# Performance work log

Measured on AMD Instinct MI355X. Metric: run time of the kernel, lower is better.

## Reference

```python
import jax, jax.numpy as jnp
import numpy as np

POS = np.array([[0,3,0.5],[0,3,1.5],[0,3,2.5],[0,3,3.5],[0,3,4.5],[0,3,5.5],[1,0,0],[1,6,6],[2,0,6],[2,6,0],[3,0,0],[3,6,6],[4,0,6],[4,6,0],[5,0,0],[5,6,6],[6,0,6],[6,6,0],[7,0,0],[7,6,6],[8,0,6],[8,6,0],[9,0,0],[9,6,6],[10,0,6],[10,6,0],[11,0,0],[11,6,6],[12,0,6],[12,6,0],[13,0,0],[13,6,6],[14,0,6],[14,6,0],[15,0,0],[15,6,6],[16,0,6],[16,6,0],[17,0.5,0.5],[17,3,0.5],[17,5.5,0.5],[17,0.5,3],[17,3,3],[17,5.5,3],[17,0.5,5.5],[17,3,5.5],[17,5.5,5.5]], dtype=np.float32)  # (47,3) fixed buffer

B, S, D, H, FF, HID = 512, 47, 32, 4, 2048, 256

def _ln(x, w, b, eps=1e-5):
    mu = jnp.mean(x, -1, keepdims=True)
    var = jnp.mean((x - mu) ** 2, -1, keepdims=True)
    return (x - mu) * jax.lax.rsqrt(var + eps) * w + b

def _encoder_layer(h, wi, bi, wo, bo, l1w, l1b, f1w, f1b, f2w, f2b, l2w, l2b):
    # torch post-norm TransformerEncoderLayer; batch_first=False => attention over axis 0
    L, N, E = h.shape
    Dh = E // H
    qkv = h @ wi.T + bi                                  # (L,N,3E)
    q, k, v = jnp.split(qkv, 3, axis=-1)
    q = q.reshape(L, N, H, Dh); k = k.reshape(L, N, H, Dh); v = v.reshape(L, N, H, Dh)
    scores = jnp.einsum('lnhd,mnhd->nhlm', q, k) * (1.0 / np.sqrt(Dh))  # (N,H,L,L)
    a = jax.nn.softmax(scores, axis=-1)
    o = jnp.einsum('nhlm,mnhd->lnhd', a, v).reshape(L, N, E)
    h = _ln(h + (o @ wo.T + bo), l1w, l1b)
    ff = jax.nn.relu(h @ f1w.T + f1b) @ f2w.T + f2b
    return _ln(h + ff, l2w, l2b)

def setup_inputs():
    key = jax.random.key(0)
    ks = list(jax.random.split(key, 24))
    rn = lambda k, s, sc=0.05: jax.random.normal(k, s, jnp.float32) * sc
    return dict(
        x=jax.random.normal(ks[0], (B, S), jnp.float32),
        w_in=rn(ks[1], (D, 1)), b_in=rn(ks[2], (D,)),
        w_pos=rn(ks[3], (D, 3)), b_pos=rn(ks[4], (D,)),
        cls_token=rn(ks[5], (1, 1, D), 1.0),
        attn_in_w=rn(ks[6], (2, 3 * D, D)), attn_in_b=rn(ks[7], (2, 3 * D)),
        attn_out_w=rn(ks[8], (2, D, D)), attn_out_b=rn(ks[9], (2, D)),
        ln1_w=jnp.ones((2, D)), ln1_b=jnp.zeros((2, D)),
        ff1_w=rn(ks[10], (2, FF, D)), ff1_b=rn(ks[11], (2, FF)),
        ff2_w=rn(ks[12], (2, D, FF)), ff2_b=rn(ks[13], (2, D)),
        ln2_w=jnp.ones((2, D)), ln2_b=jnp.zeros((2, D)),
        out_w=rn(ks[14], (1, D)), out_b=rn(ks[15], (1,)),
        mlp_w0=rn(ks[16], (HID, S)), mlp_b0=rn(ks[17], (HID,)),
        mlp_w1=rn(ks[18], (HID, HID)), mlp_b1=rn(ks[19], (HID,)),
        mlp_w2=rn(ks[20], (1, HID)), mlp_b2=rn(ks[21], (1,)),
    )

def reference(x, w_in, b_in, w_pos, b_pos, cls_token, attn_in_w, attn_in_b, attn_out_w, attn_out_b, ln1_w, ln1_b, ff1_w, ff1_b, ff2_w, ff2_b, ln2_w, ln2_b, out_w, out_b, mlp_w0, mlp_b0, mlp_w1, mlp_b1, mlp_w2, mlp_b2):
    Bn = x.shape[0]
    h = x[..., None] * w_in[:, 0] + b_in                 # Linear(1,D): (B,S,D)
    h = h + (jnp.asarray(POS) @ w_pos.T + b_pos)         # pos projection (S,D)
    cls = jnp.broadcast_to(cls_token, (Bn, 1, D))
    h = jnp.concatenate([cls, h], axis=1)                # (B,S+1,D)
    for i in range(2):
        h = _encoder_layer(h, attn_in_w[i], attn_in_b[i], attn_out_w[i], attn_out_b[i], ln1_w[i], ln1_b[i], ff1_w[i], ff1_b[i], ff2_w[i], ff2_b[i], ln2_w[i], ln2_b[i])
    out = jax.nn.relu(h[:, 1:, :] @ out_w.T + out_b)[..., 0]   # (B,S); dropout = eval identity
    o = jax.nn.relu(out @ mlp_w0.T + mlp_b0)
    o = jax.nn.relu(o @ mlp_w1.T + mlp_b1)
    o = jax.nn.relu(o @ mlp_w2.T + mlp_b2)               # MLP ends with ReLU per source
    return o
```

## Files before the change

### kernel.cpp

```cpp
#include <hip/hip_runtime.h>

#define NB 512
#define NS 47
#define NP 48
#define DIM 32
#define NFF 2048
#define NHID 256
#define NROWS (NB * NP)
#define FTOK 48

#define VSTR 520
#define PSTR 72
#define USTR 136

typedef _Float16 f16x8 __attribute__((ext_vector_type(8)));
typedef _Float16 f16x4 __attribute__((ext_vector_type(4)));
typedef float f32x4 __attribute__((ext_vector_type(4)));

__constant__ float POSC[NS * 3] = {
  0,3,0.5f, 0,3,1.5f, 0,3,2.5f, 0,3,3.5f, 0,3,4.5f, 0,3,5.5f,
  1,0,0, 1,6,6, 2,0,6, 2,6,0, 3,0,0, 3,6,6, 4,0,6, 4,6,0,
  5,0,0, 5,6,6, 6,0,6, 6,6,0, 7,0,0, 7,6,6, 8,0,6, 8,6,0,
  9,0,0, 9,6,6, 10,0,6, 10,6,0, 11,0,0, 11,6,6, 12,0,6, 12,6,0,
  13,0,0, 13,6,6, 14,0,6, 14,6,0, 15,0,0, 15,6,6, 16,0,6, 16,6,0,
  17,0.5f,0.5f, 17,3,0.5f, 17,5.5f,0.5f, 17,0.5f,3, 17,3,3, 17,5.5f,3,
  17,0.5f,5.5f, 17,3,5.5f, 17,5.5f,5.5f
};

__global__ __launch_bounds__(256) void prep16_kernel(const float* __restrict__ w1,
                                                     const float* __restrict__ w2,
                                                     _Float16* __restrict__ w1h,
                                                     _Float16* __restrict__ w2h) {
  int idx = blockIdx.x * 256 + threadIdx.x;
  w1h[idx] = (_Float16)w1[idx];
  w2h[idx] = (_Float16)w2[idx];
}

__global__ __launch_bounds__(256) void embed_kernel(
    const float* __restrict__ x, const float* __restrict__ w_in, const float* __restrict__ b_in,
    const float* __restrict__ w_pos, const float* __restrict__ b_pos,
    const float* __restrict__ cls, float* __restrict__ h) {
  int idx = blockIdx.x * 256 + threadIdx.x;
  int r = idx >> 5, d = idx & 31;
  int l = r / NP, n = r - l * NP;
  float v;
  if (n == 0) {
    v = cls[d];
  } else {
    int s = n - 1;
    v = x[l * NS + s] * w_in[d] + b_in[d]
      + POSC[s * 3 + 0] * w_pos[d * 3 + 0]
      + POSC[s * 3 + 1] * w_pos[d * 3 + 1]
      + POSC[s * 3 + 2] * w_pos[d * 3 + 2] + b_pos[d];
  }
  h[idx] = v;
}

__global__ __launch_bounds__(256) void kv_kernel(
    const float* __restrict__ h, const float* __restrict__ wi, const float* __restrict__ bi,
    _Float16* __restrict__ Kp, _Float16* __restrict__ Vt) {
  __shared__ float ws_[512];
  __shared__ float bs_[16];
  const int t = threadIdx.x;
  const int nh = blockIdx.x >> 1;
  const int n = nh >> 2, hh = nh & 3;
  const int l = ((blockIdx.x & 1) << 8) | t;
  for (int i = t; i < 512; i += 256) {
    int sub = i >> 8, rem = i & 255;
    int jj = rem >> 5, d = rem & 31;
    ws_[i] = wi[((sub + 1) * 32 + hh * 8 + jj) * 32 + d];
  }
  if (t < 16) bs_[t] = bi[((t >> 3) + 1) * 32 + hh * 8 + (t & 7)];
  __syncthreads();
  const float4* hrow = (const float4*)(h + (l * NP + n) * 32);
  float4 hv[8];
  #pragma unroll
  for (int i = 0; i < 8; ++i) hv[i] = hrow[i];
  f16x8 kh, kl_, vh;
  #pragma unroll
  for (int jj = 0; jj < 8; ++jj) {
    float k0 = bs_[jj], k1 = 0.f, k2 = 0.f, k3 = 0.f;
    float v0 = bs_[8 + jj], v1 = 0.f, v2 = 0.f, v3 = 0.f;
    #pragma unroll
    for (int d4 = 0; d4 < 8; ++d4) {
      float4 hvv = hv[d4];
      k0 += hvv.x * ws_[jj * 32 + 4 * d4 + 0];
      k1 += hvv.y * ws_[jj * 32 + 4 * d4 + 1];
      k2 += hvv.z * ws_[jj * 32 + 4 * d4 + 2];
      k3 += hvv.w * ws_[jj * 32 + 4 * d4 + 3];
      v0 += hvv.x * ws_[256 + jj * 32 + 4 * d4 + 0];
      v1 += hvv.y * ws_[256 + jj * 32 + 4 * d4 + 1];
      v2 += hvv.z * ws_[256 + jj * 32 + 4 * d4 + 2];
      v3 += hvv.w * ws_[256 + jj * 32 + 4 * d4 + 3];
    }
    float kv = (k0 + k1) + (k2 + k3);
    float vv = (v0 + v1) + (v2 + v3);
    kh[jj] = (_Float16)kv; kl_[jj] = (_Float16)(kv - (float)kh[jj]);
    vh[jj] = (_Float16)vv;
  }
  _Float16* kdst = Kp + ((size_t)nh * 512 + l) * 16;
  *(f16x8*)(kdst) = kh;
  *(f16x8*)(kdst + 8) = kl_;
  #pragma unroll
  for (int d = 0; d < 8; ++d) Vt[(size_t)nh * 4096 + d * 512 + l] = vh[d];
}

__global__ __launch_bounds__(256, 2) void attn_mfma_kernel(
    const float* __restrict__ h, const float* __restrict__ wi, const float* __restrict__ bi,
    const _Float16* __restrict__ Kp, const _Float16* __restrict__ Vt,
    float* __restrict__ o) {
  __shared__ alignas(16) _Float16 khi[512 * 8];
  __shared__ alignas(16) _Float16 klo[512 * 8];
  __shared__ alignas(16) _Float16 vts[8 * VSTR];
  __shared__ alignas(16) float hq_pls[4608];
  __shared__ alignas(16) _Float16 qf[128 * 16];
  __shared__ float wsq[256];
  __shared__ float bq[8];
  const int bx = blockIdx.x;
  const int nh = bx >> 2, qc = bx & 3;
  const int n = nh >> 2, hh = nh & 3;
  const int t = threadIdx.x;
  const int lane = t & 63, wv = t >> 6;
  const int c = lane & 15, g = lane >> 4;

  const _Float16* kg = Kp + (size_t)nh * 8192;
  for (int r = t; r < 512; r += 256) {
    const uint4* src = (const uint4*)(kg + r * 16);
    uint4 a = src[0], b = src[1];
    *(uint4*)(khi + r * 8) = a;
    *(uint4*)(klo + r * 8) = b;
  }
  {
    const _Float16* vg = Vt + (size_t)nh * 4096;
    for (int i = t; i < 512; i += 256) {
      int d = i >> 6, seg = i & 63;
      *(uint4*)(vts + d * VSTR + seg * 8) = *(const uint4*)(vg + d * 512 + seg * 8);
    }
  }
  wsq[t] = wi[(hh * 8 + (t & 7)) * 32 + (t >> 3)];
  if (t < 8) bq[t] = bi[hh * 8 + t];
  float* hq = hq_pls;

  #pragma unroll
  for (int rp = 0; rp < 2; ++rp) {
    {
      int row = t >> 2, quar = t & 3;
      const float4* src =
          (const float4*)(h + (((qc * 128 + rp * 64 + row) * NP) + n) * 32 + quar * 8);
      float4 a = src[0], b = src[1];
      __syncthreads();
      *(float4*)(hq + row * 36 + quar * 8) = a;
      *(float4*)(hq + row * 36 + quar * 8 + 4) = b;
    }
    __syncthreads();
    {
      int row = t >> 2, pr = t & 3;
      #pragma unroll
      for (int u = 0; u < 2; ++u) {
        int jj = pr * 2 + u;
        float a = bq[jj];
        #pragma unroll
        for (int d = 0; d < 32; ++d) a += hq[row * 36 + d] * wsq[d * 8 + jj];
        _Float16 qh = (_Float16)a;
        _Float16 ql = (_Float16)(a - (float)qh);
        qf[(rp * 64 + row) * 16 + jj] = qh;
        qf[(rp * 64 + row) * 16 + 8 + jj] = ql;
      }
    }
    __syncthreads();
  }

  const f16x8 hz = {(_Float16)0,(_Float16)0,(_Float16)0,(_Float16)0,
                    (_Float16)0,(_Float16)0,(_Float16)0,(_Float16)0};
  const f32x4 zf = {0.f, 0.f, 0.f, 0.f};
  _Float16* pls_ = (_Float16*)hq_pls;
  _Float16* mypA = pls_ + wv * (16 * PSTR);
  _Float16* mypB = pls_ + (4 + wv) * (16 * PSTR);
  const int q0A = qc * 128 + wv * 16;
  const int q0B = q0A + 64;

  f16x8 aqA = hz, aqB = hz;
  if (g < 3) {
    aqA = *(const f16x8*)(qf + (wv * 16 + c) * 16 + (g & 1) * 8);
    aqB = *(const f16x8*)(qf + (64 + wv * 16 + c) * 16 + (g & 1) * 8);
  }
  f32x4 accA = {0.f, 0.f, 0.f, 0.f}, accB = {0.f, 0.f, 0.f, 0.f};
  float lsA[4] = {0.f, 0.f, 0.f, 0.f}, lsB[4] = {0.f, 0.f, 0.f, 0.f};

  for (int ch = 0; ch < 8; ++ch) {
    const int kb = ch * 64;
    #pragma unroll
    for (int kt = 0; kt < 4; ++kt) {
      f16x8 bk = hz;
      if (g < 2)       bk = *(const f16x8*)(khi + (kb + kt * 16 + c) * 8);
      else if (g == 2) bk = *(const f16x8*)(klo + (kb + kt * 16 + c) * 8);
      f32x4 sA = __builtin_amdgcn_mfma_f32_16x16x32_f16(aqA, bk, zf, 0, 0, 0);
      f32x4 sB = __builtin_amdgcn_mfma_f32_16x16x32_f16(aqB, bk, zf, 0, 0, 0);
      #pragma unroll
      for (int r = 0; r < 4; ++r) {
        float pA = __expf(sA[r] * 0.35355339059327373f - 2.0f);
        float pB = __expf(sB[r] * 0.35355339059327373f - 2.0f);
        _Float16 phA = (_Float16)pA;
        _Float16 phB = (_Float16)pB;
        lsA[r] += (float)phA;
        lsB[r] += (float)phB;
        mypA[(g * 4 + r) * PSTR + kt * 16 + c] = phA;
        mypB[(g * 4 + r) * PSTR + kt * 16 + c] = phB;
      }
    }
    #pragma unroll
    for (int half = 0; half < 2; ++half) {
      f16x8 bv = hz;
      if (c < 8) bv = *(const f16x8*)(vts + c * VSTR + kb + half * 32 + g * 8);
      f16x8 apA = *(const f16x8*)(mypA + c * PSTR + half * 32 + g * 8);
      f16x8 apB = *(const f16x8*)(mypB + c * PSTR + half * 32 + g * 8);
      accA = __builtin_amdgcn_mfma_f32_16x16x32_f16(apA, bv, accA, 0, 0, 0);
      accB = __builtin_amdgcn_mfma_f32_16x16x32_f16(apB, bv, accB, 0, 0, 0);
    }
  }
  #pragma unroll
  for (int m = 1; m < 16; m <<= 1) {
    #pragma unroll
    for (int r = 0; r < 4; ++r) {
      lsA[r] += __shfl_xor(lsA[r], m, 64);
      lsB[r] += __shfl_xor(lsB[r], m, 64);
    }
  }
  if (c < 8) {
    #pragma unroll
    for (int r = 0; r < 4; ++r) {
      o[((q0A + g * 4 + r) * NP + n) * 32 + hh * 8 + c] = accA[r] / lsA[r];
      o[((q0B + g * 4 + r) * NP + n) * 32 + hh * 8 + c] = accB[r] / lsB[r];
    }
  }
}

__global__ __launch_bounds__(256) void proj_ln1_kernel(
    const float* __restrict__ o, const float* __restrict__ wo, const float* __restrict__ bo,
    const float* __restrict__ lw, const float* __restrict__ lb, float* __restrict__ h) {
  __shared__ float wos[32 * 33];
  __shared__ float pre[64 * 33];
  const int g = blockIdx.x, t = threadIdx.x;
  for (int i = t; i < 1024; i += 256) wos[(i >> 5) * 33 + (i & 31)] = wo[i];
  __syncthreads();
  const int subr = t >> 2, jq = t & 3;
  const int r = g * 64 + subr;
  const float4* orow = (const float4*)(o + r * 32);
  float4 ov[8];
  #pragma unroll
  for (int i = 0; i < 8; ++i) ov[i] = orow[i];
  const float* hres = h + r * 32 + jq * 8;
  #pragma unroll
  for (int jj = 0; jj < 8; ++jj) {
    int j = jq * 8 + jj;
    float a0 = bo[j], a1 = 0.f, a2 = 0.f, a3 = 0.f;
    #pragma unroll
    for (int d4 = 0; d4 < 8; ++d4) {
      float4 vv = ov[d4];
      a0 += vv.x * wos[j * 33 + 4 * d4 + 0];
      a1 += vv.y * wos[j * 33 + 4 * d4 + 1];
      a2 += vv.z * wos[j * 33 + 4 * d4 + 2];
      a3 += vv.w * wos[j * 33 + 4 * d4 + 3];
    }
    pre[subr * 33 + j] = (a0 + a1) + (a2 + a3) + hres[jj];
  }
  __syncthreads();
  if (t < 64) {
    float mu = 0.f;
    #pragma unroll
    for (int d = 0; d < 32; ++d) mu += pre[t * 33 + d];
    mu *= (1.f / 32.f);
    float var = 0.f;
    #pragma unroll
    for (int d = 0; d < 32; ++d) { float dv = pre[t * 33 + d] - mu; var += dv * dv; }
    float rs = rsqrtf(var * (1.f / 32.f) + 1e-5f);
    float* hrow = h + (g * 64 + t) * 32;
    #pragma unroll
    for (int d = 0; d < 32; ++d)
      hrow[d] = (pre[t * 33 + d] - mu) * rs * lw[d] + lb[d];
  }
}

__global__ __launch_bounds__(256) void ff_fused_kernel(
    const float* __restrict__ h, const _Float16* __restrict__ w1h,
    const float* __restrict__ b1, const _Float16* __restrict__ w2h,
    const float* __restrict__ b2, const float* __restrict__ lw,
    const float* __restrict__ lb, const float* __restrict__ ow,
    const float* __restrict__ ob, float* __restrict__ svec, int do_svec) {
  __shared__ alignas(16) _Float16 ubuf[4][2][16 * USTR];
  __shared__ alignas(16) float yw[4][FTOK * 33];
  const int t = threadIdx.x;
  const int lane = t & 63;
  const int wv = t >> 6;
  const int nl = lane & 15;
  const int g = lane >> 4;
  const int g4 = g * 4;
  const int r0 = blockIdx.x * FTOK;

  f16x8 hfrag[3];
  #pragma unroll
  for (int tt = 0; tt < 3; ++tt) {
    const float4 h0 = *(const float4*)(h + (r0 + tt * 16 + nl) * 32 + g * 8);
    const float4 h1 = *(const float4*)(h + (r0 + tt * 16 + nl) * 32 + g * 8 + 4);
    hfrag[tt][0] = (_Float16)h0.x; hfrag[tt][1] = (_Float16)h0.y;
    hfrag[tt][2] = (_Float16)h0.z; hfrag[tt][3] = (_Float16)h0.w;
    hfrag[tt][4] = (_Float16)h1.x; hfrag[tt][5] = (_Float16)h1.y;
    hfrag[tt][6] = (_Float16)h1.z; hfrag[tt][7] = (_Float16)h1.w;
  }

  f32x4 acc0[3] = {{0.f,0.f,0.f,0.f},{0.f,0.f,0.f,0.f},{0.f,0.f,0.f,0.f}};
  f32x4 acc1[3] = {{0.f,0.f,0.f,0.f},{0.f,0.f,0.f,0.f},{0.f,0.f,0.f,0.f}};
  const f32x4 zero = {0.f, 0.f, 0.f, 0.f};
  const int ffbase = wv * 512;

  #pragma unroll
  for (int sc = 0; sc < 4; ++sc) {
    const int ffb = ffbase + sc * 128;
    f16x8 wf[8];
    float4 bv[8];
    #pragma unroll
    for (int ft = 0; ft < 8; ++ft) {
      wf[ft] = *(const f16x8*)(w1h + (ffb + ft * 16 + nl) * 32 + g * 8);
      bv[ft] = *(const float4*)(b1 + ffb + ft * 16 + g4);
    }
    f16x8 w2f0[4], w2f1[4];
    #pragma unroll
    for (int kk = 0; kk < 4; ++kk) {
      w2f0[kk] = *(const f16x8*)(w2h + nl * NFF + ffb + kk * 32 + g * 8);
      w2f1[kk] = *(const f16x8*)(w2h + (16 + nl) * NFF + ffb + kk * 32 + g * 8);
    }
    #pragma unroll
    for (int tt = 0; tt < 3; ++tt) {
      _Float16* ub = ubuf[wv][tt & 1];
      f32x4 cc[8];
      #pragma unroll
      for (int ft = 0; ft < 8; ++ft)
        cc[ft] = __builtin_amdgcn_mfma_f32_16x16x32_f16(wf[ft], hfrag[tt], zero, 0, 0, 0);
      #pragma unroll
      for (int ft = 0; ft < 8; ++ft) {
        f16x4 uv;
        uv[0] = (_Float16)fmaxf(cc[ft][0] + bv[ft].x, 0.f);
        uv[1] = (_Float16)fmaxf(cc[ft][1] + bv[ft].y, 0.f);
        uv[2] = (_Float16)fmaxf(cc[ft][2] + bv[ft].z, 0.f);
        uv[3] = (_Float16)fmaxf(cc[ft][3] + bv[ft].w, 0.f);
        *(f16x4*)(ub + nl * USTR + ft * 16 + g4) = uv;
      }
      #pragma unroll
      for (int kk = 0; kk < 4; ++kk) {
        f16x8 uf = *(const f16x8*)(ub + nl * USTR + kk * 32 + g * 8);
        acc0[tt] = __builtin_amdgcn_mfma_f32_16x16x32_f16(uf, w2f0[kk], acc0[tt], 0, 0, 0);
        acc1[tt] = __builtin_amdgcn_mfma_f32_16x16x32_f16(uf, w2f1[kk], acc1[tt], 0, 0, 0);
      }
    }
  }
  #pragma unroll
  for (int tt = 0; tt < 3; ++tt) {
    #pragma unroll
    for (int r = 0; r < 4; ++r) {
      yw[wv][(tt * 16 + g4 + r) * 33 + nl]      = acc0[tt][r];
      yw[wv][(tt * 16 + g4 + r) * 33 + 16 + nl] = acc1[tt][r];
    }
  }
  __syncthreads();

  float* pre = (float*)ubuf;
  {
    int idx = t;
    #pragma unroll
    for (int u = 0; u < 6; ++u, idx += 256) {
      int tok = idx >> 5, d = idx & 31;
      int off = tok * 33 + d;
      float v = yw[0][off] + yw[1][off] + yw[2][off] + yw[3][off]
              + b2[d] + h[(r0 + tok) * 32 + d];
      pre[off] = v;
    }
  }
  __syncthreads();

  if (t < FTOK) {
    float mu = 0.f;
    #pragma unroll
    for (int d = 0; d < 32; ++d) mu += pre[t * 33 + d];
    mu *= (1.f / 32.f);
    float var = 0.f;
    #pragma unroll
    for (int d = 0; d < 32; ++d) { float dv = pre[t * 33 + d] - mu; var += dv * dv; }
    float rs = rsqrtf(var * (1.f / 32.f) + 1e-5f);
    const int rr = r0 + t;
    float* hrow = (float*)h + (size_t)rr * 32;
    float hn[32];
    #pragma unroll
    for (int d = 0; d < 32; ++d) {
      hn[d] = (pre[t * 33 + d] - mu) * rs * lw[d] + lb[d];
      hrow[d] = hn[d];
    }
    if (do_svec) {
      int l = rr / NP, n = rr - l * NP;
      if (n > 0) {
        float a = ob[0];
        #pragma unroll
        for (int d = 0; d < 32; ++d) a += hn[d] * ow[d];
        svec[l * NS + (n - 1)] = fmaxf(a, 0.f);
      }
    }
  }
}

__global__ __launch_bounds__(256) void head_kernel(
    const float* __restrict__ svec,
    const float* __restrict__ m0w, const float* __restrict__ m0b,
    const float* __restrict__ m1w, const float* __restrict__ m1b,
    const float* __restrict__ m2w, const float* __restrict__ m2b,
    float* __restrict__ out) {
  __shared__ float sv[NS];
  __shared__ float hid[NHID];
  __shared__ float red[4];
  const int l = blockIdx.x, t = threadIdx.x;
  if (t < NS) sv[t] = svec[l * NS + t];
  __syncthreads();
  {
    float a = m0b[t];
    const float* wr = m0w + t * NS;
    #pragma unroll
    for (int s = 0; s < NS; ++s) a += sv[s] * wr[s];
    hid[t] = fmaxf(a, 0.f);
  }
  __syncthreads();
  {
    float a = m1b[t];
    const float4* wr = (const float4*)(m1w + t * NHID);
    #pragma unroll 8
    for (int j4 = 0; j4 < 64; ++j4) {
      float4 w = wr[j4];
      a += hid[4 * j4 + 0] * w.x + hid[4 * j4 + 1] * w.y
         + hid[4 * j4 + 2] * w.z + hid[4 * j4 + 3] * w.w;
    }
    float h2 = fmaxf(a, 0.f);
    float part = h2 * m2w[t];
    #pragma unroll
    for (int off = 32; off > 0; off >>= 1) part += __shfl_down(part, off, 64);
    if ((t & 63) == 0) red[t >> 6] = part;
  }
  __syncthreads();
  if (t == 0) out[l] = fmaxf(red[0] + red[1] + red[2] + red[3] + m2b[0], 0.f);
}

extern "C" void kernel_launch(void* const* d_in, const int* in_sizes, int n_in,
                              void* d_out, int out_size, void* d_ws, size_t ws_size,
                              hipStream_t stream) {
  (void)in_sizes; (void)n_in; (void)out_size; (void)ws_size;
  const float* x     = (const float*)d_in[0];
  const float* w_in  = (const float*)d_in[1];
  const float* b_in  = (const float*)d_in[2];
  const float* w_pos = (const float*)d_in[3];
  const float* b_pos = (const float*)d_in[4];
  const float* cls   = (const float*)d_in[5];
  const float* wi    = (const float*)d_in[6];
  const float* bi    = (const float*)d_in[7];
  const float* wo    = (const float*)d_in[8];
  const float* bo    = (const float*)d_in[9];
  const float* l1w   = (const float*)d_in[10];
  const float* l1b   = (const float*)d_in[11];
  const float* f1w   = (const float*)d_in[12];
  const float* f1b   = (const float*)d_in[13];
  const float* f2w   = (const float*)d_in[14];
  const float* f2b   = (const float*)d_in[15];
  const float* l2w   = (const float*)d_in[16];
  const float* l2b   = (const float*)d_in[17];
  const float* ow    = (const float*)d_in[18];
  const float* ob    = (const float*)d_in[19];
  const float* m0w   = (const float*)d_in[20];
  const float* m0b   = (const float*)d_in[21];
  const float* m1w   = (const float*)d_in[22];
  const float* m1b   = (const float*)d_in[23];
  const float* m2w   = (const float*)d_in[24];
  const float* m2b   = (const float*)d_in[25];
  float* out = (float*)d_out;

  float* ws   = (float*)d_ws;
  float* h    = ws;
  float* o    = ws + 786432;
  float* R2   = ws + 1572864;
  _Float16* Kp = (_Float16*)R2;
  _Float16* Vt = (_Float16*)(R2 + 786432);
  float* svec = ws + 2752512;
  _Float16* w1h = (_Float16*)(ws + 2776576);
  _Float16* w2h = (_Float16*)(ws + 2842112);

  prep16_kernel<<<512, 256, 0, stream>>>(f1w, f2w, w1h, w2h);
  embed_kernel<<<3072, 256, 0, stream>>>(x, w_in, b_in, w_pos, b_pos, cls, h);
  for (int L = 0; L < 2; ++L) {
    kv_kernel<<<384, 256, 0, stream>>>(h, wi + L * 3072, bi + L * 96, Kp, Vt);
    attn_mfma_kernel<<<768, 256, 0, stream>>>(h, wi + L * 3072, bi + L * 96, Kp, Vt, o);
    proj_ln1_kernel<<<384, 256, 0, stream>>>(o, wo + L * 1024, bo + L * 32,
                                             l1w + L * 32, l1b + L * 32, h);
    ff_fused_kernel<<<512, 256, 0, stream>>>(h, w1h + L * 65536, f1b + L * NFF,
                                             w2h + L * 65536, f2b + L * 32,
                                             l2w + L * 32, l2b + L * 32,
                                             ow, ob, svec, L);
  }
  head_kernel<<<512, 256, 0, stream>>>(svec, m0w, m0b, m1w, m1b, m2w, m2b, out);
}
```

Before: 157.5 us.

## Double FF tokens per block and merge weight prep with embedding kernel

```diff
diff --git a/kernel.cpp b/kernel.cpp
--- a/kernel.cpp
+++ b/kernel.cpp
@@ -7,7 +7,7 @@
 #define NFF 2048
 #define NHID 256
 #define NROWS (NB * NP)
-#define FTOK 48
+#define FTOK 96
 
 #define VSTR 520
 #define PSTR 72
@@ -27,20 +27,21 @@
   17,0.5f,5.5f, 17,3,5.5f, 17,5.5f,5.5f
 };
 
-__global__ __launch_bounds__(256) void prep16_kernel(const float* __restrict__ w1,
-                                                     const float* __restrict__ w2,
-                                                     _Float16* __restrict__ w1h,
-                                                     _Float16* __restrict__ w2h) {
-  int idx = blockIdx.x * 256 + threadIdx.x;
-  w1h[idx] = (_Float16)w1[idx];
-  w2h[idx] = (_Float16)w2[idx];
-}
-
-__global__ __launch_bounds__(256) void embed_kernel(
-    const float* __restrict__ x, const float* __restrict__ w_in, const float* __restrict__ b_in,
-    const float* __restrict__ w_pos, const float* __restrict__ b_pos,
-    const float* __restrict__ cls, float* __restrict__ h) {
-  int idx = blockIdx.x * 256 + threadIdx.x;
+__global__ __launch_bounds__(256) void prep_embed_kernel(
+    const float* __restrict__ w1, const float* __restrict__ w2,
+    _Float16* __restrict__ w1h, _Float16* __restrict__ w2h,
+    const float* __restrict__ x, const float* __restrict__ w_in,
+    const float* __restrict__ b_in, const float* __restrict__ w_pos,
+    const float* __restrict__ b_pos, const float* __restrict__ cls,
+    float* __restrict__ h) {
+  const int bx = blockIdx.x;
+  if (bx < 512) {
+    int idx = bx * 256 + threadIdx.x;
+    w1h[idx] = (_Float16)w1[idx];
+    w2h[idx] = (_Float16)w2[idx];
+    return;
+  }
+  int idx = (bx - 512) * 256 + threadIdx.x;
   int r = idx >> 5, d = idx & 31;
   int l = r / NP, n = r - l * NP;
   float v;
@@ -297,9 +298,9 @@
   const int g4 = g * 4;
   const int r0 = blockIdx.x * FTOK;
 
-  f16x8 hfrag[3];
-  #pragma unroll
-  for (int tt = 0; tt < 3; ++tt) {
+  f16x8 hfrag[6];
+  #pragma unroll
+  for (int tt = 0; tt < 6; ++tt) {
     const float4 h0 = *(const float4*)(h + (r0 + tt * 16 + nl) * 32 + g * 8);
     const float4 h1 = *(const float4*)(h + (r0 + tt * 16 + nl) * 32 + g * 8 + 4);
     hfrag[tt][0] = (_Float16)h0.x; hfrag[tt][1] = (_Float16)h0.y;
@@ -308,8 +309,12 @@
     hfrag[tt][6] = (_Float16)h1.z; hfrag[tt][7] = (_Float16)h1.w;
   }
 
-  f32x4 acc0[3] = {{0.f,0.f,0.f,0.f},{0.f,0.f,0.f,0.f},{0.f,0.f,0.f,0.f}};
-  f32x4 acc1[3] = {{0.f,0.f,0.f,0.f},{0.f,0.f,0.f,0.f},{0.f,0.f,0.f,0.f}};
+  f32x4 acc0[6], acc1[6];
+  #pragma unroll
+  for (int tt = 0; tt < 6; ++tt) {
+    acc0[tt] = (f32x4){0.f, 0.f, 0.f, 0.f};
+    acc1[tt] = (f32x4){0.f, 0.f, 0.f, 0.f};
+  }
   const f32x4 zero = {0.f, 0.f, 0.f, 0.f};
   const int ffbase = wv * 512;
 
@@ -330,7 +335,7 @@
       w2f1[kk] = *(const f16x8*)(w2h + (16 + nl) * NFF + ffb + kk * 32 + g * 8);
     }
     #pragma unroll
-    for (int tt = 0; tt < 3; ++tt) {
+    for (int tt = 0; tt < 6; ++tt) {
       _Float16* ub = ubuf[wv][tt & 1];
       f32x4 cc[8];
       #pragma unroll
@@ -354,7 +359,7 @@
     }
   }
   #pragma unroll
-  for (int tt = 0; tt < 3; ++tt) {
+  for (int tt = 0; tt < 6; ++tt) {
     #pragma unroll
     for (int r = 0; r < 4; ++r) {
       yw[wv][(tt * 16 + g4 + r) * 33 + nl]      = acc0[tt][r];
@@ -367,7 +372,7 @@
   {
     int idx = t;
     #pragma unroll
-    for (int u = 0; u < 6; ++u, idx += 256) {
+    for (int u = 0; u < 12; ++u, idx += 256) {
       int tok = idx >> 5, d = idx & 31;
       int off = tok * 33 + d;
       float v = yw[0][off] + yw[1][off] + yw[2][off] + yw[3][off]
@@ -487,14 +492,14 @@
   _Float16* w1h = (_Float16*)(ws + 2776576);
   _Float16* w2h = (_Float16*)(ws + 2842112);
 
-  prep16_kernel<<<512, 256, 0, stream>>>(f1w, f2w, w1h, w2h);
-  embed_kernel<<<3072, 256, 0, stream>>>(x, w_in, b_in, w_pos, b_pos, cls, h);
+  prep_embed_kernel<<<3584, 256, 0, stream>>>(f1w, f2w, w1h, w2h,
+                                              x, w_in, b_in, w_pos, b_pos, cls, h);
   for (int L = 0; L < 2; ++L) {
     kv_kernel<<<384, 256, 0, stream>>>(h, wi + L * 3072, bi + L * 96, Kp, Vt);
     attn_mfma_kernel<<<768, 256, 0, stream>>>(h, wi + L * 3072, bi + L * 96, Kp, Vt, o);
     proj_ln1_kernel<<<384, 256, 0, stream>>>(o, wo + L * 1024, bo + L * 32,
                                              l1w + L * 32, l1b + L * 32, h);
-    ff_fused_kernel<<<512, 256, 0, stream>>>(h, w1h + L * 65536, f1b + L * NFF,
+    ff_fused_kernel<<<256, 256, 0, stream>>>(h, w1h + L * 65536, f1b + L * NFF,
                                              w2h + L * 65536, f2b + L * 32,
                                              l2w + L * 32, l2b + L * 32,
                                              ow, ob, svec, L);
```

Result: no change. 154.9 us (-1.6%).
